# Performance work log

Measured on AMD Instinct MI355X. Metric: run time of the kernel, lower is better.

Reference implementation:

```python
import jax, jax.numpy as jnp
import numpy as np

N = 100_000      # n_nodes
E = 1_600_000    # n_edges (avg degree 16)
D_IN, D_H, D_OUT = 128, 128, 64
SIM_THRESH = 0.1


def setup_inputs() -> dict:
    key = jax.random.key(0)
    k = jax.random.split(key, 6)
    row = jax.random.randint(k[0], (E,), 0, N, dtype=jnp.int32)
    off = jax.random.randint(k[1], (E,), 1, N, dtype=jnp.int32)
    col = ((row + off) % N).astype(jnp.int32)  # guarantees no self-loops
    edge_index = jnp.stack([row, col], axis=0)
    x = jax.random.normal(k[2], (N, D_IN), dtype=jnp.float32)
    W1 = jax.random.normal(k[3], (D_IN, D_H), dtype=jnp.float32) / np.sqrt(D_IN)
    b1 = jnp.zeros((D_H,), jnp.float32)
    W2 = jax.random.normal(k[4], (D_H, D_OUT), dtype=jnp.float32) / np.sqrt(D_H)
    b2 = jnp.zeros((D_OUT,), jnp.float32)
    return {"x": x, "edge_index": edge_index, "W1": W1, "b1": b1, "W2": W2, "b2": b2}


def _att_coef(x, row, col, valid):
    """Edge-wise cosine-similarity attention (GNNGuard att_coef), fixed edge set.
    valid: bool [E] mask of edges still alive (pass-1 pruning).
    Returns per-edge weight w [E] (0 for pruned edges), per-node self-loop
    weight w_self [N], and the surviving-edge mask."""
    # cosine similarity per edge (never materialize NxN)
    xn = x / jnp.maximum(jnp.linalg.norm(x, axis=1, keepdims=True), 1e-12)
    sim = jnp.einsum('ed,ed->e', xn[row], xn[col])           # [E]
    sim = jnp.where(sim < SIM_THRESH, 0.0, sim)
    sim = jnp.where(valid, sim, 0.0)
    # L1 row normalization (segment reduce over destination rows)
    rowsum = jax.ops.segment_sum(sim, row, num_segments=N)   # [N]
    rs = rowsum[row]
    att = jnp.where(rs > 0, sim / jnp.where(rs > 0, rs, 1.0), 0.0)
    nz = att > 0                                             # edges kept by sparse matrix
    # degree-based self-loop weight: lam = 1/(deg+1)
    deg = jax.ops.segment_sum(nz.astype(x.dtype), row, num_segments=N)
    lam = 1.0 / (deg + 1.0)
    # exponentiate only stored (nonzero) entries, matching scipy sparse semantics
    w = jnp.where(nz, jnp.exp(att), 0.0)                     # [E]
    w_self = jnp.exp(lam)                                    # [N]
    return w, w_self, nz


def _gcn_conv(x, row, col, w, w_self, W, b):
    """GCNConv with given edge weights + self-loop weights, symmetric norm."""
    h = x @ W                                                # [N, d_out]
    deg = jax.ops.segment_sum(w, row, num_segments=N) + w_self
    dinv = jnp.where(deg > 0, jax.lax.rsqrt(deg), 0.0)       # deg^-1/2
    we = dinv[row] * w * dinv[col]                           # [E]
    agg = jax.ops.segment_sum(we[:, None] * h[col], row, num_segments=N)
    agg = agg + (w_self * dinv * dinv)[:, None] * h          # self-loop term
    return agg + b


def reference(x, edge_index, W1, b1, W2, b2):
    row, col = edge_index[0], edge_index[1]
    all_valid = jnp.ones((E,), dtype=bool)
    # attention pass 1 on raw features
    w1e, w1s, nz1 = _att_coef(x, row, col, all_valid)
    h = jax.nn.relu(_gcn_conv(x, row, col, w1e, w1s, W1, b1))
    # attention pass 2 on hidden features, restricted to surviving edges
    # (self-loops added in pass 1 are stripped again before re-normalization)
    w2e, w2s, _ = _att_coef(h, row, col, nz1)
    # dropout is identity at inference (training=False)
    out = _gcn_conv(h, row, col, w2e, w2s, W2, b2)
    return jax.nn.log_softmax(out, axis=1)
```

## Files before the change

kernel.cpp:

```cpp
#include <hip/hip_runtime.h>
#include <math.h>

#define SIM_THRESH 0.1f
#define Q_SCREEN_THRESH 0.07f

__global__ void norms_q_kernel(const float* __restrict__ x, float* __restrict__ norm,
                               char* __restrict__ qn, int n) {
  int gid = blockIdx.x * blockDim.x + threadIdx.x;
  int r = gid >> 6, lane = gid & 63;
  if (r >= n) return;
  float2 v = ((const float2*)(x + (size_t)r * 128))[lane];
  float s = v.x * v.x + v.y * v.y;
#pragma unroll
  for (int o = 1; o < 64; o <<= 1) s += __shfl_xor(s, o);
  float nr = sqrtf(s);
  if (lane == 0) norm[r] = nr;
  float inv = 127.f / fmaxf(nr, 1e-12f);
  int qa = (int)rintf(v.x * inv);
  int qb = (int)rintf(v.y * inv);
  unsigned short packed = (unsigned short)((qa & 0xff) | ((qb & 0xff) << 8));
  *(unsigned short*)(qn + (size_t)r * 128 + lane * 2) = packed;
}

static __device__ __forceinline__ int dot4i8(int a, int b, int acc) {
#if __has_builtin(__builtin_amdgcn_sdot4)
  return __builtin_amdgcn_sdot4(a, b, acc, false);
#else
  const char4 av = *(const char4*)&a;
  const char4 bv = *(const char4*)&b;
  return acc + (int)av.x * bv.x + (int)av.y * bv.y + (int)av.z * bv.z + (int)av.w * bv.w;
#endif
}

template <int DOUT>
__global__ void __launch_bounds__(256) gemm_kernel(const float* __restrict__ X,
                                                   const float* __restrict__ W,
                                                   float* __restrict__ out, int n) {
  constexpr int BM = 128, BK = 32;
  constexpr int TN = DOUT / 16;
  constexpr int XS = BK + 4;
  constexpr int WS = DOUT + 4;
  __shared__ float Xs[BM * XS];
  __shared__ float Ws[BK * WS];

  const int t = threadIdx.x;
  const int tx = t & 15;
  const int ty = t >> 4;
  const int base = blockIdx.x * BM;

  float acc[8][TN];
#pragma unroll
  for (int i = 0; i < 8; ++i)
#pragma unroll
    for (int j = 0; j < TN; ++j) acc[i][j] = 0.f;

  const int lr = t >> 3;
  const int lk4 = (t & 7) * 4;
  constexpr int F4R = DOUT / 4;
  constexpr int KSTEP = 256 / F4R;
  const int wc = t % F4R;
  const int wk0 = t / F4R;

  for (int kb = 0; kb < 128; kb += BK) {
    __syncthreads();
#pragma unroll
    for (int j = 0; j < 4; ++j) {
      int r = lr + 32 * j;
      int gr = base + r;
      float4 v = make_float4(0.f, 0.f, 0.f, 0.f);
      if (gr < n) v = *(const float4*)(X + (size_t)gr * 128 + kb + lk4);
      *(float4*)(Xs + r * XS + lk4) = v;
    }
#pragma unroll
    for (int k = wk0; k < BK; k += KSTEP) {
      float4 v = *(const float4*)(W + (size_t)(kb + k) * DOUT + wc * 4);
      *(float4*)(Ws + k * WS + wc * 4) = v;
    }
    __syncthreads();

#pragma unroll
    for (int k4 = 0; k4 < BK; k4 += 4) {
      float4 xf[8];
#pragma unroll
      for (int i = 0; i < 8; ++i) xf[i] = *(const float4*)(Xs + (ty + 16 * i) * XS + k4);
      float4 wf[4][TN / 4];
#pragma unroll
      for (int kk = 0; kk < 4; ++kk)
#pragma unroll
        for (int jj = 0; jj < TN / 4; ++jj)
          wf[kk][jj] = *(const float4*)(Ws + (k4 + kk) * WS + tx * TN + jj * 4);
#pragma unroll
      for (int i = 0; i < 8; ++i) {
        const float xk[4] = {xf[i].x, xf[i].y, xf[i].z, xf[i].w};
#pragma unroll
        for (int kk = 0; kk < 4; ++kk) {
#pragma unroll
          for (int jj = 0; jj < TN / 4; ++jj) {
            acc[i][jj * 4 + 0] = fmaf(xk[kk], wf[kk][jj].x, acc[i][jj * 4 + 0]);
            acc[i][jj * 4 + 1] = fmaf(xk[kk], wf[kk][jj].y, acc[i][jj * 4 + 1]);
            acc[i][jj * 4 + 2] = fmaf(xk[kk], wf[kk][jj].z, acc[i][jj * 4 + 2]);
            acc[i][jj * 4 + 3] = fmaf(xk[kk], wf[kk][jj].w, acc[i][jj * 4 + 3]);
          }
        }
      }
    }
  }

#pragma unroll
  for (int i = 0; i < 8; ++i) {
    int gr = base + ty + 16 * i;
    if (gr < n) {
#pragma unroll
      for (int jj = 0; jj < TN / 4; ++jj) {
        float4 v = make_float4(acc[i][jj * 4 + 0], acc[i][jj * 4 + 1], acc[i][jj * 4 + 2],
                               acc[i][jj * 4 + 3]);
        *(float4*)(out + (size_t)gr * DOUT + tx * TN + jj * 4) = v;
      }
    }
  }
}

__global__ void sim1_kernel(const char* __restrict__ qn, const float* __restrict__ x,
                            const float* __restrict__ norm, const int* __restrict__ row,
                            const int* __restrict__ col, float* __restrict__ sim,
                            int* __restrict__ cnt, int e) {
  int gid = blockIdx.x * blockDim.x + threadIdx.x;
  int p = gid >> 4, l = gid & 15;
  if (p >= e) return;
  int r = row[p], c = col[p];
  int2 qa = *(const int2*)(qn + (size_t)r * 128 + l * 8);
  int2 qb = *(const int2*)(qn + (size_t)c * 128 + l * 8);
  int si = 0;
  si = dot4i8(qa.x, qb.x, si);
  si = dot4i8(qa.y, qb.y, si);
#pragma unroll
  for (int o = 1; o < 16; o <<= 1) si += __shfl_xor(si, o);
  float v = (float)si * (1.f / 16129.f);
  if (v > Q_SCREEN_THRESH) {
    const float4* fr = (const float4*)(x + (size_t)r * 128) + 2 * l;
    const float4* fc = (const float4*)(x + (size_t)c * 128) + 2 * l;
    float4 a0 = fr[0], a1 = fr[1], b0 = fc[0], b1 = fc[1];
    float t = a0.x * b0.x + a0.y * b0.y + a0.z * b0.z + a0.w * b0.w + a1.x * b1.x + a1.y * b1.y +
              a1.z * b1.z + a1.w * b1.w;
#pragma unroll
    for (int o = 1; o < 16; o <<= 1) t += __shfl_xor(t, o);
    float nr = fmaxf(norm[r], 1e-12f), nc = fmaxf(norm[c], 1e-12f);
    v = t / (nr * nc);
  } else {
    v = 0.f;
  }
  if (l == 0) {
    v = (v < SIM_THRESH) ? 0.f : v;
    sim[p] = v;
    if (v > 0.f) atomicAdd(&cnt[r], 1);
  }
}

__global__ void scan1_kernel(const int* __restrict__ cnt, int* __restrict__ excl,
                             int* __restrict__ bsum, int n) {
  __shared__ int sd[256];
  int t = threadIdx.x;
  int base = blockIdx.x * 1024 + t * 4;
  int v[4];
  int s = 0;
#pragma unroll
  for (int k = 0; k < 4; k++) {
    int idx = base + k;
    v[k] = (idx < n) ? cnt[idx] : 0;
    s += v[k];
  }
  sd[t] = s;
  __syncthreads();
  for (int off = 1; off < 256; off <<= 1) {
    int tmp = (t >= off) ? sd[t - off] : 0;
    __syncthreads();
    sd[t] += tmp;
    __syncthreads();
  }
  int ex = sd[t] - s;
#pragma unroll
  for (int k = 0; k < 4; k++) {
    int idx = base + k;
    if (idx < n) excl[idx] = ex;
    ex += v[k];
  }
  if (t == 255) bsum[blockIdx.x] = sd[255];
}

__global__ void scan2_kernel(int* __restrict__ bsum, int nb, int* __restrict__ total_out) {
  if (threadIdx.x == 0 && blockIdx.x == 0) {
    int acc = 0;
    for (int i = 0; i < nb; i++) {
      int v = bsum[i];
      bsum[i] = acc;
      acc += v;
    }
    *total_out = acc;
  }
}

__global__ void scan3_kernel(int* __restrict__ excl, const int* __restrict__ bsum, int n) {
  int i = blockIdx.x * 1024 + threadIdx.x;
  if (i < n) excl[i] += bsum[blockIdx.x];
}

__global__ void fillc_kernel(const int* __restrict__ row, const int* __restrict__ col,
                             const float* __restrict__ sim, const int* __restrict__ rp,
                             int* __restrict__ cur, int4* __restrict__ rec, int e) {
  int i = blockIdx.x * blockDim.x + threadIdx.x;
  if (i < e) {
    float s = sim[i];
    if (s > 0.f) {
      int r = row[i];
      int p = rp[r] + atomicAdd(&cur[r], 1);
      int4 v;
      v.x = r;
      v.y = col[i];
      v.z = __float_as_int(s);
      v.w = 0;
      rec[p] = v;
    }
  }
}

__global__ void row_att1_kernel(const int* __restrict__ rp, const int4* __restrict__ rec,
                                float* __restrict__ w, float* __restrict__ wself,
                                float* __restrict__ dinv, int n) {
  int r = blockIdx.x * blockDim.x + threadIdx.x;
  if (r >= n) return;
  int s0 = rp[r], s1 = rp[r + 1];
  float rs = 0.f;
  for (int p = s0; p < s1; p++) rs += __int_as_float(rec[p].z);
  float degw = 0.f;
  for (int p = s0; p < s1; p++) {
    float wv = expf(__int_as_float(rec[p].z) / rs);
    w[p] = wv;
    degw += wv;
  }
  float ws = expf(1.f / (float)(s1 - s0 + 1));
  degw += ws;
  wself[r] = ws;
  dinv[r] = 1.f / sqrtf(degw);
}

__global__ void agg_relu_norm_kernel(const float* __restrict__ hin, const int* __restrict__ rp,
                                     const int4* __restrict__ rec, const float* __restrict__ w,
                                     const float* __restrict__ wself,
                                     const float* __restrict__ dinv,
                                     const float* __restrict__ bias, float* __restrict__ hout,
                                     float* __restrict__ normout, int n) {
  int gid = blockIdx.x * blockDim.x + threadIdx.x;
  int r = gid >> 6, lane = gid & 63;
  if (r >= n) return;
  float di = dinv[r];
  float2 acc = {0.f, 0.f};
  int s0 = rp[r], s1 = rp[r + 1];
  for (int p = s0; p < s1; p++) {
    int c = rec[p].y;
    float we = di * w[p] * dinv[c];
    float2 hv = ((const float2*)(hin + (size_t)c * 128))[lane];
    acc.x = fmaf(we, hv.x, acc.x);
    acc.y = fmaf(we, hv.y, acc.y);
  }
  float self = wself[r] * di * di;
  float2 hr = ((const float2*)(hin + (size_t)r * 128))[lane];
  float2 bv = ((const float2*)bias)[lane];
  acc.x = fmaf(self, hr.x, acc.x) + bv.x;
  acc.y = fmaf(self, hr.y, acc.y) + bv.y;
  acc.x = fmaxf(acc.x, 0.f);
  acc.y = fmaxf(acc.y, 0.f);
  ((float2*)(hout + (size_t)r * 128))[lane] = acc;
  float s = acc.x * acc.x + acc.y * acc.y;
#pragma unroll
  for (int o = 1; o < 64; o <<= 1) s += __shfl_xor(s, o);
  if (lane == 0) normout[r] = sqrtf(s);
}

__global__ void sim2_kernel(const float* __restrict__ h, const float* __restrict__ norm,
                            const int4* __restrict__ rec, const int* __restrict__ nnz_p,
                            float* __restrict__ sim2) {
  int nnz = *nnz_p;
  int tid = blockIdx.x * blockDim.x + threadIdx.x;
  int ngroups = (gridDim.x * blockDim.x) >> 4;
  int g = tid >> 4, l = tid & 15;
  for (int p = g; p < nnz; p += ngroups) {
    int4 rv = rec[p];
    int r = rv.x, c = rv.y;
    const float4* fr = (const float4*)(h + (size_t)r * 128) + 2 * l;
    const float4* fc = (const float4*)(h + (size_t)c * 128) + 2 * l;
    float4 a0 = fr[0], a1 = fr[1], b0 = fc[0], b1 = fc[1];
    float s = a0.x * b0.x + a0.y * b0.y + a0.z * b0.z + a0.w * b0.w + a1.x * b1.x + a1.y * b1.y +
              a1.z * b1.z + a1.w * b1.w;
#pragma unroll
    for (int o = 1; o < 16; o <<= 1) s += __shfl_xor(s, o);
    if (l == 0) {
      float nr = fmaxf(norm[r], 1e-12f), nc = fmaxf(norm[c], 1e-12f);
      float v = s / (nr * nc);
      sim2[p] = (v < SIM_THRESH) ? 0.f : v;
    }
  }
}

__global__ void row_att2_kernel(const int* __restrict__ rp, const float* __restrict__ sim2,
                                float* __restrict__ w, float* __restrict__ wself,
                                float* __restrict__ dinv, int n) {
  int r = blockIdx.x * blockDim.x + threadIdx.x;
  if (r >= n) return;
  int s0 = rp[r], s1 = rp[r + 1];
  float rs = 0.f;
  int cnt2 = 0;
  for (int p = s0; p < s1; p++) {
    float sv = sim2[p];
    rs += sv;
    if (sv > 0.f) cnt2++;
  }
  float degw = 0.f;
  for (int p = s0; p < s1; p++) {
    float sv = sim2[p];
    float wv = (sv > 0.f) ? expf(sv / rs) : 0.f;
    w[p] = wv;
    degw += wv;
  }
  float ws = expf(1.f / (float)(cnt2 + 1));
  degw += ws;
  wself[r] = ws;
  dinv[r] = 1.f / sqrtf(degw);
}

__global__ void agg2_lsm_kernel(const float* __restrict__ hin, const int* __restrict__ rp,
                                const int4* __restrict__ rec, const float* __restrict__ w,
                                const float* __restrict__ wself, const float* __restrict__ dinv,
                                const float* __restrict__ bias, float* __restrict__ out, int n) {
  int gid = blockIdx.x * blockDim.x + threadIdx.x;
  int r = gid >> 6, lane = gid & 63;
  if (r >= n) return;
  float di = dinv[r];
  float acc = 0.f;
  int s0 = rp[r], s1 = rp[r + 1];
  for (int p = s0; p < s1; p++) {
    float wv = w[p];
    if (wv > 0.f) {
      int c = rec[p].y;
      acc = fmaf(di * wv * dinv[c], hin[(size_t)c * 64 + lane], acc);
    }
  }
  acc += wself[r] * di * di * hin[(size_t)r * 64 + lane] + bias[lane];
  float m = acc;
#pragma unroll
  for (int o = 1; o < 64; o <<= 1) m = fmaxf(m, __shfl_xor(m, o));
  float ex = expf(acc - m);
  float ssum = ex;
#pragma unroll
  for (int o = 1; o < 64; o <<= 1) ssum += __shfl_xor(ssum, o);
  out[(size_t)r * 64 + lane] = acc - m - logf(ssum);
}

extern "C" void kernel_launch(void* const* d_in, const int* in_sizes, int n_in, void* d_out,
                              int out_size, void* d_ws, size_t ws_size, hipStream_t stream) {
  const float* x = (const float*)d_in[0];
  const int* ei = (const int*)d_in[1];
  const float* W1 = (const float*)d_in[2];
  const float* b1 = (const float*)d_in[3];
  const float* W2 = (const float*)d_in[4];
  const float* b2 = (const float*)d_in[5];
  const int n = in_sizes[0] / 128;
  const int e = in_sizes[1] / 2;
  const int* row = ei;
  const int* col = ei + e;

  char* ws = (char*)d_ws;
  size_t off = 0;
  auto alloc = [&](size_t bytes) -> char* {
    char* p = ws + off;
    off = (off + bytes + 511) & ~(size_t)511;
    return p;
  };
  float* h1 = (float*)alloc((size_t)n * 128 * 4);
  float* h = (float*)alloc((size_t)n * 128 * 4);
  int4* rec = (int4*)alloc((size_t)e * 16);
  float* recf = (float*)rec;
  char* qn = (char*)rec;
  float* wbuf = recf + (size_t)2 * e;
  float* sim2b = recf + (size_t)3 * e;
  float* simb = h;
  int* rp = (int*)alloc((size_t)(n + 1) * 4);
  int* cnt = (int*)alloc((size_t)n * 4);
  int* cur = (int*)alloc((size_t)n * 4);
  float* norm = (float*)alloc((size_t)n * 4);
  float* wself = (float*)alloc((size_t)n * 4);
  float* dinv = (float*)alloc((size_t)n * 4);
  const int nb = (n + 1023) / 1024;
  int* bsum = (int*)alloc((size_t)nb * 4);
  float* h2 = h1;
  float* out = (float*)d_out;

  hipMemsetAsync(cnt, 0, (size_t)n * 4, stream);
  hipMemsetAsync(cur, 0, (size_t)n * 4, stream);

  const int gblocks = (n + 127) / 128;
  norms_q_kernel<<<(n * 64 + 255) / 256, 256, 0, stream>>>(x, norm, qn, n);
  gemm_kernel<128><<<gblocks, 256, 0, stream>>>(x, W1, h1, n);
  sim1_kernel<<<(e * 16 + 255) / 256, 256, 0, stream>>>(qn, x, norm, row, col, simb, cnt, e);
  scan1_kernel<<<nb, 256, 0, stream>>>(cnt, rp, bsum, n);
  scan2_kernel<<<1, 64, 0, stream>>>(bsum, nb, rp + n);
  scan3_kernel<<<nb, 1024, 0, stream>>>(rp, bsum, n);
  fillc_kernel<<<(e + 255) / 256, 256, 0, stream>>>(row, col, simb, rp, cur, rec, e);
  row_att1_kernel<<<(n + 255) / 256, 256, 0, stream>>>(rp, rec, wbuf, wself, dinv, n);
  agg_relu_norm_kernel<<<(n * 64 + 255) / 256, 256, 0, stream>>>(h1, rp, rec, wbuf, wself, dinv,
                                                                 b1, h, norm, n);
  sim2_kernel<<<4096, 256, 0, stream>>>(h, norm, rec, rp + n, sim2b);
  row_att2_kernel<<<(n + 255) / 256, 256, 0, stream>>>(rp, sim2b, wbuf, wself, dinv, n);
  gemm_kernel<64><<<gblocks, 256, 0, stream>>>(h, W2, h2, n);
  agg2_lsm_kernel<<<(n * 64 + 255) / 256, 256, 0, stream>>>(h2, rp, rec, wbuf, wself, dinv, b2,
                                                            out, n);
}
```

Measured before the change: 384.9 us.

## Co-schedule GEMMs with similarity kernels in fused launches and raise screen threshold

Merges the first GEMM with the sim1 edge kernel, and the second GEMM with the sim2 kernel, into single launches where the leading blocks do GEMM tiles and the rest do edge similarity. The aim is to overlap compute-bound GEMM work with memory-bound gathers and to drop launch gaps. It also shrinks the GEMM K-tile to 16 to save shared memory, adds nontemporal loads and stores for streaming edge arrays, and raises the int8 screening threshold so fewer edges need the exact fp32 recheck. The higher screen threshold risks rejecting edges whose true similarity is just above 0.1.

```diff
diff --git a/kernel.cpp b/kernel.cpp
--- a/kernel.cpp
+++ b/kernel.cpp
@@ -2,7 +2,17 @@
 #include <math.h>
 
 #define SIM_THRESH 0.1f
-#define Q_SCREEN_THRESH 0.07f
+#define Q_SCREEN_THRESH 0.085f
+
+static __device__ __forceinline__ int dot4i8(int a, int b, int acc) {
+#if __has_builtin(__builtin_amdgcn_sdot4)
+  return __builtin_amdgcn_sdot4(a, b, acc, false);
+#else
+  const char4 av = *(const char4*)&a;
+  const char4 bv = *(const char4*)&b;
+  return acc + (int)av.x * bv.x + (int)av.y * bv.y + (int)av.z * bv.z + (int)av.w * bv.w;
+#endif
+}
 
 __global__ void norms_q_kernel(const float* __restrict__ x, float* __restrict__ norm,
                                char* __restrict__ qn, int n) {
@@ -22,31 +32,20 @@
   *(unsigned short*)(qn + (size_t)r * 128 + lane * 2) = packed;
 }
 
-static __device__ __forceinline__ int dot4i8(int a, int b, int acc) {
-#if __has_builtin(__builtin_amdgcn_sdot4)
-  return __builtin_amdgcn_sdot4(a, b, acc, false);
-#else
-  const char4 av = *(const char4*)&a;
-  const char4 bv = *(const char4*)&b;
-  return acc + (int)av.x * bv.x + (int)av.y * bv.y + (int)av.z * bv.z + (int)av.w * bv.w;
-#endif
-}
-
-template <int DOUT>
-__global__ void __launch_bounds__(256) gemm_kernel(const float* __restrict__ X,
-                                                   const float* __restrict__ W,
-                                                   float* __restrict__ out, int n) {
-  constexpr int BM = 128, BK = 32;
+template <int DOUT, int BK>
+__device__ __forceinline__ void gemm_body(const float* __restrict__ X,
+                                          const float* __restrict__ W, float* __restrict__ out,
+                                          int n, int bid, int t) {
+  constexpr int BM = 128;
   constexpr int TN = DOUT / 16;
   constexpr int XS = BK + 4;
   constexpr int WS = DOUT + 4;
   __shared__ float Xs[BM * XS];
   __shared__ float Ws[BK * WS];
 
-  const int t = threadIdx.x;
   const int tx = t & 15;
   const int ty = t >> 4;
-  const int base = blockIdx.x * BM;
+  const int base = bid * BM;
 
   float acc[8][TN];
 #pragma unroll
@@ -54,8 +53,10 @@
 #pragma unroll
     for (int j = 0; j < TN; ++j) acc[i][j] = 0.f;
 
-  const int lr = t >> 3;
-  const int lk4 = (t & 7) * 4;
+  constexpr int F4X = BK / 4;
+  constexpr int XROWS = 256 / F4X;
+  const int xr = t / F4X;
+  const int xc4 = (t % F4X) * 4;
   constexpr int F4R = DOUT / 4;
   constexpr int KSTEP = 256 / F4R;
   const int wc = t % F4R;
@@ -64,12 +65,12 @@
   for (int kb = 0; kb < 128; kb += BK) {
     __syncthreads();
 #pragma unroll
-    for (int j = 0; j < 4; ++j) {
-      int r = lr + 32 * j;
+    for (int j = 0; j < BM / XROWS; ++j) {
+      int r = xr + XROWS * j;
       int gr = base + r;
       float4 v = make_float4(0.f, 0.f, 0.f, 0.f);
-      if (gr < n) v = *(const float4*)(X + (size_t)gr * 128 + kb + lk4);
-      *(float4*)(Xs + r * XS + lk4) = v;
+      if (gr < n) v = *(const float4*)(X + (size_t)gr * 128 + kb + xc4);
+      *(float4*)(Xs + r * XS + xc4) = v;
     }
 #pragma unroll
     for (int k = wk0; k < BK; k += KSTEP) {
@@ -120,14 +121,20 @@
   }
 }
 
-__global__ void sim1_kernel(const char* __restrict__ qn, const float* __restrict__ x,
-                            const float* __restrict__ norm, const int* __restrict__ row,
-                            const int* __restrict__ col, float* __restrict__ sim,
-                            int* __restrict__ cnt, int e) {
-  int gid = blockIdx.x * blockDim.x + threadIdx.x;
+__global__ void __launch_bounds__(256) fused_g128_sim1(
+    const float* __restrict__ X, const float* __restrict__ W1, float* __restrict__ h1, int n,
+    int gb, const char* __restrict__ qn, const float* __restrict__ x,
+    const float* __restrict__ norm, const int* __restrict__ row, const int* __restrict__ col,
+    float* __restrict__ sim, int* __restrict__ cnt, int e) {
+  if ((int)blockIdx.x < gb) {
+    gemm_body<128, 16>(X, W1, h1, n, blockIdx.x, threadIdx.x);
+    return;
+  }
+  int gid = (blockIdx.x - gb) * 256 + threadIdx.x;
   int p = gid >> 4, l = gid & 15;
   if (p >= e) return;
-  int r = row[p], c = col[p];
+  int r = __builtin_nontemporal_load(row + p);
+  int c = __builtin_nontemporal_load(col + p);
   int2 qa = *(const int2*)(qn + (size_t)r * 128 + l * 8);
   int2 qb = *(const int2*)(qn + (size_t)c * 128 + l * 8);
   int si = 0;
@@ -151,7 +158,7 @@
   }
   if (l == 0) {
     v = (v < SIM_THRESH) ? 0.f : v;
-    sim[p] = v;
+    __builtin_nontemporal_store(v, sim + p);
     if (v > 0.f) atomicAdd(&cnt[r], 1);
   }
 }
@@ -209,13 +216,14 @@
                              int* __restrict__ cur, int4* __restrict__ rec, int e) {
   int i = blockIdx.x * blockDim.x + threadIdx.x;
   if (i < e) {
-    float s = sim[i];
+    float s = __builtin_nontemporal_load(sim + i);
     if (s > 0.f) {
-      int r = row[i];
+      int r = __builtin_nontemporal_load(row + i);
+      int cc = __builtin_nontemporal_load(col + i);
       int p = rp[r] + atomicAdd(&cur[r], 1);
       int4 v;
       v.x = r;
-      v.y = col[i];
+      v.y = cc;
       v.z = __float_as_int(s);
       v.w = 0;
       rec[p] = v;
@@ -276,14 +284,20 @@
   if (lane == 0) normout[r] = sqrtf(s);
 }
 
-__global__ void sim2_kernel(const float* __restrict__ h, const float* __restrict__ norm,
-                            const int4* __restrict__ rec, const int* __restrict__ nnz_p,
-                            float* __restrict__ sim2) {
+__global__ void __launch_bounds__(256) fused_g64_sim2(
+    const float* __restrict__ h, const float* __restrict__ W2, float* __restrict__ h2, int n,
+    int gb, const float* __restrict__ norm, const int4* __restrict__ rec,
+    const int* __restrict__ nnz_p, float* __restrict__ sim2, int sb) {
+  if ((int)blockIdx.x < gb) {
+    gemm_body<64, 16>(h, W2, h2, n, blockIdx.x, threadIdx.x);
+    return;
+  }
+  int sid = blockIdx.x - gb;
   int nnz = *nnz_p;
-  int tid = blockIdx.x * blockDim.x + threadIdx.x;
-  int ngroups = (gridDim.x * blockDim.x) >> 4;
-  int g = tid >> 4, l = tid & 15;
-  for (int p = g; p < nnz; p += ngroups) {
+  int g = sid * 16 + (threadIdx.x >> 4);
+  int l = threadIdx.x & 15;
+  int stride = sb * 16;
+  for (int p = g; p < nnz; p += stride) {
     int4 rv = rec[p];
     int r = rv.x, c = rv.y;
     const float4* fr = (const float4*)(h + (size_t)r * 128) + 2 * l;
@@ -397,10 +411,13 @@
   hipMemsetAsync(cnt, 0, (size_t)n * 4, stream);
   hipMemsetAsync(cur, 0, (size_t)n * 4, stream);
 
-  const int gblocks = (n + 127) / 128;
+  const int gb = (n + 127) / 128;
+  const int sb1 = (e * 16 + 255) / 256;
+  const int sb2 = 4096;
+
   norms_q_kernel<<<(n * 64 + 255) / 256, 256, 0, stream>>>(x, norm, qn, n);
-  gemm_kernel<128><<<gblocks, 256, 0, stream>>>(x, W1, h1, n);
-  sim1_kernel<<<(e * 16 + 255) / 256, 256, 0, stream>>>(qn, x, norm, row, col, simb, cnt, e);
+  fused_g128_sim1<<<gb + sb1, 256, 0, stream>>>(x, W1, h1, n, gb, qn, x, norm, row, col, simb,
+                                                cnt, e);
   scan1_kernel<<<nb, 256, 0, stream>>>(cnt, rp, bsum, n);
   scan2_kernel<<<1, 64, 0, stream>>>(bsum, nb, rp + n);
   scan3_kernel<<<nb, 1024, 0, stream>>>(rp, bsum, n);
@@ -408,9 +425,8 @@
   row_att1_kernel<<<(n + 255) / 256, 256, 0, stream>>>(rp, rec, wbuf, wself, dinv, n);
   agg_relu_norm_kernel<<<(n * 64 + 255) / 256, 256, 0, stream>>>(h1, rp, rec, wbuf, wself, dinv,
                                                                  b1, h, norm, n);
-  sim2_kernel<<<4096, 256, 0, stream>>>(h, norm, rec, rp + n, sim2b);
+  fused_g64_sim2<<<gb + sb2, 256, 0, stream>>>(h, W2, h2, n, gb, norm, rec, rp + n, sim2b, sb2);
   row_att2_kernel<<<(n + 255) / 256, 256, 0, stream>>>(rp, sim2b, wbuf, wself, dinv, n);
-  gemm_kernel<64><<<gblocks, 256, 0, stream>>>(h, W2, h2, n);
   agg2_lsm_kernel<<<(n * 64 + 255) / 256, 256, 0, stream>>>(h2, rp, rec, wbuf, wself, dinv, b2,
                                                             out, n);
 }
```

Measured after the change: 503.9 us. 30.9% more time.

## Split int8 screening into separate pass and add int8 screening to pass-2 similarity

Applied to the files above, without the earlier changes.

Pass-1 similarity is split into a compact int8 screen kernel that writes a byte mask, followed by an fp32 recompute kernel that only does work for edges passing the screen. The screen threshold is raised. The aggregation kernel now also emits int8-quantized hidden features, which sim2 uses to skip the fp32 dot product for clearly dissimilar edges. This adds a memset, extra kernels and scratch aliasing (mask aliases the weight buffer, qn2 aliases the output). The approximate screen risks dropping edges whose true similarity sits just above the threshold.

```diff
diff --git a/kernel.cpp b/kernel.cpp
--- a/kernel.cpp
+++ b/kernel.cpp
@@ -2,7 +2,17 @@
 #include <math.h>
 
 #define SIM_THRESH 0.1f
-#define Q_SCREEN_THRESH 0.07f
+#define Q_SCREEN_THRESH 0.085f
+
+static __device__ __forceinline__ int dot4i8(int a, int b, int acc) {
+#if __has_builtin(__builtin_amdgcn_sdot4)
+  return __builtin_amdgcn_sdot4(a, b, acc, false);
+#else
+  const char4 av = *(const char4*)&a;
+  const char4 bv = *(const char4*)&b;
+  return acc + (int)av.x * bv.x + (int)av.y * bv.y + (int)av.z * bv.z + (int)av.w * bv.w;
+#endif
+}
 
 __global__ void norms_q_kernel(const float* __restrict__ x, float* __restrict__ norm,
                                char* __restrict__ qn, int n) {
@@ -20,16 +30,6 @@
   int qb = (int)rintf(v.y * inv);
   unsigned short packed = (unsigned short)((qa & 0xff) | ((qb & 0xff) << 8));
   *(unsigned short*)(qn + (size_t)r * 128 + lane * 2) = packed;
-}
-
-static __device__ __forceinline__ int dot4i8(int a, int b, int acc) {
-#if __has_builtin(__builtin_amdgcn_sdot4)
-  return __builtin_amdgcn_sdot4(a, b, acc, false);
-#else
-  const char4 av = *(const char4*)&a;
-  const char4 bv = *(const char4*)&b;
-  return acc + (int)av.x * bv.x + (int)av.y * bv.y + (int)av.z * bv.z + (int)av.w * bv.w;
-#endif
 }
 
 template <int DOUT>
@@ -120,39 +120,51 @@
   }
 }
 
-__global__ void sim1_kernel(const char* __restrict__ qn, const float* __restrict__ x,
-                            const float* __restrict__ norm, const int* __restrict__ row,
-                            const int* __restrict__ col, float* __restrict__ sim,
-                            int* __restrict__ cnt, int e) {
+__global__ void screen1_kernel(const char* __restrict__ qn, const int* __restrict__ row,
+                               const int* __restrict__ col, unsigned char* __restrict__ mask,
+                               int e) {
+  int gid = blockIdx.x * blockDim.x + threadIdx.x;
+  int p = gid >> 3, l = gid & 7;
+  if (p >= e) return;
+  int r = __builtin_nontemporal_load(row + p);
+  int c = __builtin_nontemporal_load(col + p);
+  int4 qa = *(const int4*)(qn + (size_t)r * 128 + l * 16);
+  int4 qb = *(const int4*)(qn + (size_t)c * 128 + l * 16);
+  int si = dot4i8(qa.x, qb.x, 0);
+  si = dot4i8(qa.y, qb.y, si);
+  si = dot4i8(qa.z, qb.z, si);
+  si = dot4i8(qa.w, qb.w, si);
+#pragma unroll
+  for (int o = 1; o < 8; o <<= 1) si += __shfl_xor(si, o);
+  if (l == 0) {
+    float v = (float)si * (1.f / 16129.f);
+    mask[p] = (v > Q_SCREEN_THRESH) ? (unsigned char)1 : (unsigned char)0;
+  }
+}
+
+__global__ void recompute1_kernel(const unsigned char* __restrict__ mask,
+                                  const float* __restrict__ x, const float* __restrict__ norm,
+                                  const int* __restrict__ row, const int* __restrict__ col,
+                                  float* __restrict__ sim, int* __restrict__ cnt, int e) {
   int gid = blockIdx.x * blockDim.x + threadIdx.x;
   int p = gid >> 4, l = gid & 15;
   if (p >= e) return;
+  if (!mask[p]) return;
   int r = row[p], c = col[p];
-  int2 qa = *(const int2*)(qn + (size_t)r * 128 + l * 8);
-  int2 qb = *(const int2*)(qn + (size_t)c * 128 + l * 8);
-  int si = 0;
-  si = dot4i8(qa.x, qb.x, si);
-  si = dot4i8(qa.y, qb.y, si);
-#pragma unroll
-  for (int o = 1; o < 16; o <<= 1) si += __shfl_xor(si, o);
-  float v = (float)si * (1.f / 16129.f);
-  if (v > Q_SCREEN_THRESH) {
-    const float4* fr = (const float4*)(x + (size_t)r * 128) + 2 * l;
-    const float4* fc = (const float4*)(x + (size_t)c * 128) + 2 * l;
-    float4 a0 = fr[0], a1 = fr[1], b0 = fc[0], b1 = fc[1];
-    float t = a0.x * b0.x + a0.y * b0.y + a0.z * b0.z + a0.w * b0.w + a1.x * b1.x + a1.y * b1.y +
-              a1.z * b1.z + a1.w * b1.w;
-#pragma unroll
-    for (int o = 1; o < 16; o <<= 1) t += __shfl_xor(t, o);
+  const float4* fr = (const float4*)(x + (size_t)r * 128) + 2 * l;
+  const float4* fc = (const float4*)(x + (size_t)c * 128) + 2 * l;
+  float4 a0 = fr[0], a1 = fr[1], b0 = fc[0], b1 = fc[1];
+  float t = a0.x * b0.x + a0.y * b0.y + a0.z * b0.z + a0.w * b0.w + a1.x * b1.x + a1.y * b1.y +
+            a1.z * b1.z + a1.w * b1.w;
+#pragma unroll
+  for (int o = 1; o < 16; o <<= 1) t += __shfl_xor(t, o);
+  if (l == 0) {
     float nr = fmaxf(norm[r], 1e-12f), nc = fmaxf(norm[c], 1e-12f);
-    v = t / (nr * nc);
-  } else {
-    v = 0.f;
-  }
-  if (l == 0) {
-    v = (v < SIM_THRESH) ? 0.f : v;
-    sim[p] = v;
-    if (v > 0.f) atomicAdd(&cnt[r], 1);
+    float v = t / (nr * nc);
+    if (v >= SIM_THRESH) {
+      sim[p] = v;
+      atomicAdd(&cnt[r], 1);
+    }
   }
 }
 
@@ -204,22 +216,24 @@
   if (i < n) excl[i] += bsum[blockIdx.x];
 }
 
-__global__ void fillc_kernel(const int* __restrict__ row, const int* __restrict__ col,
-                             const float* __restrict__ sim, const int* __restrict__ rp,
-                             int* __restrict__ cur, int4* __restrict__ rec, int e) {
+__global__ void fillc_kernel(const unsigned char* __restrict__ mask, const int* __restrict__ row,
+                             const int* __restrict__ col, const float* __restrict__ sim,
+                             const int* __restrict__ rp, int* __restrict__ cur,
+                             int4* __restrict__ rec, int e) {
   int i = blockIdx.x * blockDim.x + threadIdx.x;
-  if (i < e) {
-    float s = sim[i];
-    if (s > 0.f) {
-      int r = row[i];
-      int p = rp[r] + atomicAdd(&cur[r], 1);
-      int4 v;
-      v.x = r;
-      v.y = col[i];
-      v.z = __float_as_int(s);
-      v.w = 0;
-      rec[p] = v;
-    }
+  if (i >= e) return;
+  if (!mask[i]) return;
+  float s = sim[i];
+  if (s > 0.f) {
+    int r = row[i];
+    int cc = col[i];
+    int p = rp[r] + atomicAdd(&cur[r], 1);
+    int4 v;
+    v.x = r;
+    v.y = cc;
+    v.z = __float_as_int(s);
+    v.w = 0;
+    rec[p] = v;
   }
 }
 
@@ -248,7 +262,7 @@
                                      const float* __restrict__ wself,
                                      const float* __restrict__ dinv,
                                      const float* __restrict__ bias, float* __restrict__ hout,
-                                     float* __restrict__ normout, int n) {
+                                     float* __restrict__ normout, char* __restrict__ qn2, int n) {
   int gid = blockIdx.x * blockDim.x + threadIdx.x;
   int r = gid >> 6, lane = gid & 63;
   if (r >= n) return;
@@ -273,12 +287,18 @@
   float s = acc.x * acc.x + acc.y * acc.y;
 #pragma unroll
   for (int o = 1; o < 64; o <<= 1) s += __shfl_xor(s, o);
-  if (lane == 0) normout[r] = sqrtf(s);
+  float nrm = sqrtf(s);
+  if (lane == 0) normout[r] = nrm;
+  float inv = 127.f / fmaxf(nrm, 1e-12f);
+  int qa = (int)rintf(acc.x * inv);
+  int qb = (int)rintf(acc.y * inv);
+  *(unsigned short*)(qn2 + (size_t)r * 128 + lane * 2) =
+      (unsigned short)((qa & 0xff) | ((qb & 0xff) << 8));
 }
 
 __global__ void sim2_kernel(const float* __restrict__ h, const float* __restrict__ norm,
-                            const int4* __restrict__ rec, const int* __restrict__ nnz_p,
-                            float* __restrict__ sim2) {
+                            const char* __restrict__ qn2, const int4* __restrict__ rec,
+                            const int* __restrict__ nnz_p, float* __restrict__ sim2) {
   int nnz = *nnz_p;
   int tid = blockIdx.x * blockDim.x + threadIdx.x;
   int ngroups = (gridDim.x * blockDim.x) >> 4;
@@ -286,18 +306,27 @@
   for (int p = g; p < nnz; p += ngroups) {
     int4 rv = rec[p];
     int r = rv.x, c = rv.y;
-    const float4* fr = (const float4*)(h + (size_t)r * 128) + 2 * l;
-    const float4* fc = (const float4*)(h + (size_t)c * 128) + 2 * l;
-    float4 a0 = fr[0], a1 = fr[1], b0 = fc[0], b1 = fc[1];
-    float s = a0.x * b0.x + a0.y * b0.y + a0.z * b0.z + a0.w * b0.w + a1.x * b1.x + a1.y * b1.y +
-              a1.z * b1.z + a1.w * b1.w;
-#pragma unroll
-    for (int o = 1; o < 16; o <<= 1) s += __shfl_xor(s, o);
-    if (l == 0) {
+    int2 qa = *(const int2*)(qn2 + (size_t)r * 128 + l * 8);
+    int2 qb = *(const int2*)(qn2 + (size_t)c * 128 + l * 8);
+    int si = dot4i8(qa.x, qb.x, 0);
+    si = dot4i8(qa.y, qb.y, si);
+#pragma unroll
+    for (int o = 1; o < 16; o <<= 1) si += __shfl_xor(si, o);
+    float v;
+    if ((float)si * (1.f / 16129.f) > Q_SCREEN_THRESH) {
+      const float4* fr = (const float4*)(h + (size_t)r * 128) + 2 * l;
+      const float4* fc = (const float4*)(h + (size_t)c * 128) + 2 * l;
+      float4 a0 = fr[0], a1 = fr[1], b0 = fc[0], b1 = fc[1];
+      float s = a0.x * b0.x + a0.y * b0.y + a0.z * b0.z + a0.w * b0.w + a1.x * b1.x +
+                a1.y * b1.y + a1.z * b1.z + a1.w * b1.w;
+#pragma unroll
+      for (int o = 1; o < 16; o <<= 1) s += __shfl_xor(s, o);
       float nr = fmaxf(norm[r], 1e-12f), nc = fmaxf(norm[c], 1e-12f);
-      float v = s / (nr * nc);
-      sim2[p] = (v < SIM_THRESH) ? 0.f : v;
-    }
+      v = s / (nr * nc);
+    } else {
+      v = 0.f;
+    }
+    if (l == 0) sim2[p] = (v < SIM_THRESH) ? 0.f : v;
   }
 }
 
@@ -380,6 +409,7 @@
   int4* rec = (int4*)alloc((size_t)e * 16);
   float* recf = (float*)rec;
   char* qn = (char*)rec;
+  unsigned char* mask = (unsigned char*)(recf + (size_t)2 * e);
   float* wbuf = recf + (size_t)2 * e;
   float* sim2b = recf + (size_t)3 * e;
   float* simb = h;
@@ -393,22 +423,26 @@
   int* bsum = (int*)alloc((size_t)nb * 4);
   float* h2 = h1;
   float* out = (float*)d_out;
+  char* qn2 = (char*)d_out;
 
   hipMemsetAsync(cnt, 0, (size_t)n * 4, stream);
   hipMemsetAsync(cur, 0, (size_t)n * 4, stream);
+  hipMemsetAsync(simb, 0, (size_t)e * 4, stream);
 
   const int gblocks = (n + 127) / 128;
   norms_q_kernel<<<(n * 64 + 255) / 256, 256, 0, stream>>>(x, norm, qn, n);
   gemm_kernel<128><<<gblocks, 256, 0, stream>>>(x, W1, h1, n);
-  sim1_kernel<<<(e * 16 + 255) / 256, 256, 0, stream>>>(qn, x, norm, row, col, simb, cnt, e);
+  screen1_kernel<<<(e * 8 + 255) / 256, 256, 0, stream>>>(qn, row, col, mask, e);
+  recompute1_kernel<<<(e * 16 + 255) / 256, 256, 0, stream>>>(mask, x, norm, row, col, simb,
+                                                              cnt, e);
   scan1_kernel<<<nb, 256, 0, stream>>>(cnt, rp, bsum, n);
   scan2_kernel<<<1, 64, 0, stream>>>(bsum, nb, rp + n);
   scan3_kernel<<<nb, 1024, 0, stream>>>(rp, bsum, n);
-  fillc_kernel<<<(e + 255) / 256, 256, 0, stream>>>(row, col, simb, rp, cur, rec, e);
+  fillc_kernel<<<(e + 255) / 256, 256, 0, stream>>>(mask, row, col, simb, rp, cur, rec, e);
   row_att1_kernel<<<(n + 255) / 256, 256, 0, stream>>>(rp, rec, wbuf, wself, dinv, n);
   agg_relu_norm_kernel<<<(n * 64 + 255) / 256, 256, 0, stream>>>(h1, rp, rec, wbuf, wself, dinv,
-                                                                 b1, h, norm, n);
-  sim2_kernel<<<4096, 256, 0, stream>>>(h, norm, rec, rp + n, sim2b);
+                                                                 b1, h, norm, qn2, n);
+  sim2_kernel<<<4096, 256, 0, stream>>>(h, norm, qn2, rec, rp + n, sim2b);
   row_att2_kernel<<<(n + 255) / 256, 256, 0, stream>>>(rp, sim2b, wbuf, wself, dinv, n);
   gemm_kernel<64><<<gblocks, 256, 0, stream>>>(h, W2, h2, n);
   agg2_lsm_kernel<<<(n * 64 + 255) / 256, 256, 0, stream>>>(h2, rp, rec, wbuf, wself, dinv, b2,
```

New measurement: 422.4 us. +9.8%, slower.
